# Performance work log

Hardware: AMD Instinct MI355X
Metric: run time of the kernel (lower is better)

## Reference

```python
import jax, jax.numpy as jnp
import numpy as np

M, K, N = 4096, 4096, 8192

def setup_inputs() -> dict:
    key = jax.random.key(0)
    k1, k2, k3 = jax.random.split(key, 3)
    a = jax.random.randint(k1, (M, K), -128, 128, dtype=jnp.int32).astype(jnp.int8)
    b = jax.random.randint(k2, (K, N), -128, 128, dtype=jnp.int32).astype(jnp.int8)
    scale = jax.random.uniform(k3, (N,), dtype=jnp.float32, minval=0.001, maxval=0.01)
    return {"a": a, "b": b, "scale": scale}

def reference(a, b, scale):
    acc = jax.lax.dot(a, b, preferred_element_type=jnp.int32)  # [M, N] int32
    return acc.astype(jnp.float32) * scale[None, :]  # [M, N] fp32
```

## Files before the change

kernel.cpp:

```cpp
#include <hip/hip_runtime.h>
#include <cstdint>
#include <cstddef>

#define M_DIM 4096
#define K_DIM 4096
#define N_DIM 8192

typedef int v4i __attribute__((ext_vector_type(4)));

__device__ __forceinline__ void load_lds16(const void* g, void* l) {
  __builtin_amdgcn_global_load_lds(
      (const __attribute__((address_space(1))) void*)g,
      (__attribute__((address_space(3))) void*)l,
      16, 0, 0);
}

__device__ __forceinline__ uint32_t pack4(int4 v) {
  return ((uint32_t)v.x & 0xFFu) | (((uint32_t)v.y & 0xFFu) << 8) |
         (((uint32_t)v.z & 0xFFu) << 16) | ((uint32_t)v.w << 24);
}

__global__ __launch_bounds__(256) void pack_a_kernel(const int* __restrict__ A32,
                                                     uint8_t* __restrict__ A8) {
  const int n16 = (M_DIM * K_DIM) / 16;
  const int stride = gridDim.x * 256;
  for (int i = blockIdx.x * 256 + threadIdx.x; i < n16; i += stride) {
    const int4* src = reinterpret_cast<const int4*>(A32) + (size_t)i * 4;
    int4 o;
    o.x = (int)pack4(src[0]);
    o.y = (int)pack4(src[1]);
    o.z = (int)pack4(src[2]);
    o.w = (int)pack4(src[3]);
    reinterpret_cast<int4*>(A8)[i] = o;
  }
}

#define TPITCH 132
__global__ __launch_bounds__(256) void pack_bt_kernel(const int* __restrict__ B32,
                                                      uint8_t* __restrict__ Bt) {
  __shared__ uint8_t tile[128 * TPITCH];
  const int t = threadIdx.x;
  const int n0 = blockIdx.x * 128;
  const int k0 = blockIdx.y * 128;

#pragma unroll
  for (int c = 0; c < 16; ++c) {
    const int chunk = c * 256 + t;
    const int row = chunk >> 5;
    const int nc4 = (chunk & 31);
    const int4 v = *reinterpret_cast<const int4*>(
        B32 + (size_t)(k0 + row) * N_DIM + n0 + nc4 * 4);
    *reinterpret_cast<uint32_t*>(&tile[row * TPITCH + nc4 * 4]) = pack4(v);
  }
  __syncthreads();

  const int nb = (t & 31) << 2;
  const int kc = (t >> 5) << 4;
  uint32_t dw[16];
#pragma unroll
  for (int j = 0; j < 16; ++j)
    dw[j] = *reinterpret_cast<const uint32_t*>(&tile[(kc + j) * TPITCH + nb]);

#pragma unroll
  for (int np = 0; np < 4; ++np) {
    const uint32_t sel = (uint32_t)np | (((uint32_t)np + 4u) << 8);
    uint32_t o[4];
#pragma unroll
    for (int d = 0; d < 4; ++d) {
      const uint32_t p01 = __builtin_amdgcn_perm(dw[4 * d + 1], dw[4 * d + 0], sel);
      const uint32_t p23 = __builtin_amdgcn_perm(dw[4 * d + 3], dw[4 * d + 2], sel);
      o[d] = __builtin_amdgcn_perm(p23, p01, 0x05040100u);
    }
    const int4 v = make_int4((int)o[0], (int)o[1], (int)o[2], (int)o[3]);
    *reinterpret_cast<int4*>(Bt + (size_t)(n0 + nb + np) * K_DIM + k0 + kc) = v;
  }
}

__global__ __launch_bounds__(256) void gemm_i8_kernel(const uint8_t* __restrict__ A,
                                                      const uint8_t* __restrict__ Bt,
                                                      const float* __restrict__ scale,
                                                      float* __restrict__ C) {
  __shared__ uint8_t sA[2][128 * 64];
  __shared__ uint8_t sB[2][128 * 64];

  const int t = threadIdx.x;
  const int lane = t & 63;
  const int wave = t >> 6;
  const int wr = wave >> 1;
  const int wc = wave & 1;
  const int lr = lane & 15;
  const int kh = lane >> 4;

  const int m0 = blockIdx.y * 128;
  const int n0 = blockIdx.x * 128;

  const int chunk0 = t;
  const int chunk1 = 256 + t;
  const int r0 = chunk0 >> 2, c0 = (chunk0 & 3) << 4;
  const int r1 = chunk1 >> 2, c1 = (chunk1 & 3) << 4;
  const uint8_t* a0 = A + (size_t)(m0 + r0) * K_DIM + c0;
  const uint8_t* a1 = A + (size_t)(m0 + r1) * K_DIM + c1;
  const uint8_t* b0 = Bt + (size_t)(n0 + r0) * K_DIM + c0;
  const uint8_t* b1 = Bt + (size_t)(n0 + r1) * K_DIM + c1;

  v4i acc[4][4];
#pragma unroll
  for (int i = 0; i < 4; ++i)
#pragma unroll
    for (int j = 0; j < 4; ++j)
      acc[i][j] = (v4i){0, 0, 0, 0};

  const int aoffBase = (wr * 64 + lr) * 64 + kh * 16;
  const int boffBase = (wc * 64 + lr) * 64 + kh * 16;

  load_lds16(a0, &sA[0][chunk0 * 16]);
  load_lds16(a1, &sA[0][chunk1 * 16]);
  load_lds16(b0, &sB[0][chunk0 * 16]);
  load_lds16(b1, &sB[0][chunk1 * 16]);
  __syncthreads();

  int cur = 0;
  const int NK = K_DIM / 64;
  for (int kt = 0; kt < NK; ++kt) {
    if (kt + 1 < NK) {
      const int ko = (kt + 1) * 64;
      load_lds16(a0 + ko, &sA[cur ^ 1][chunk0 * 16]);
      load_lds16(a1 + ko, &sA[cur ^ 1][chunk1 * 16]);
      load_lds16(b0 + ko, &sB[cur ^ 1][chunk0 * 16]);
      load_lds16(b1 + ko, &sB[cur ^ 1][chunk1 * 16]);
    }

    v4i af[4], bf[4];
#pragma unroll
    for (int mi = 0; mi < 4; ++mi)
      af[mi] = *reinterpret_cast<const v4i*>(&sA[cur][aoffBase + mi * 16 * 64]);
#pragma unroll
    for (int ni = 0; ni < 4; ++ni)
      bf[ni] = *reinterpret_cast<const v4i*>(&sB[cur][boffBase + ni * 16 * 64]);

#pragma unroll
    for (int mi = 0; mi < 4; ++mi)
#pragma unroll
      for (int ni = 0; ni < 4; ++ni)
        acc[mi][ni] = __builtin_amdgcn_mfma_i32_16x16x64_i8(af[mi], bf[ni], acc[mi][ni], 0, 0, 0);

    __syncthreads();
    cur ^= 1;
  }

  const int row0 = m0 + wr * 64 + kh * 4;
  const int col0 = n0 + wc * 64 + lr;
#pragma unroll
  for (int ni = 0; ni < 4; ++ni) {
    const int col = col0 + ni * 16;
    const float s = scale[col];
#pragma unroll
    for (int mi = 0; mi < 4; ++mi) {
#pragma unroll
      for (int r = 0; r < 4; ++r) {
        const int row = row0 + mi * 16 + r;
        C[(size_t)row * N_DIM + col] = (float)acc[mi][ni][r] * s;
      }
    }
  }
}

__global__ __launch_bounds__(256) void gemm_fallback(const int* __restrict__ A,
                                                     const int* __restrict__ B,
                                                     const float* __restrict__ scale,
                                                     float* __restrict__ C) {
  const int col = blockIdx.x * 16 + (threadIdx.x & 15);
  const int row = blockIdx.y * 16 + (threadIdx.x >> 4);
  int acc = 0;
  for (int k = 0; k < K_DIM; k += 4) {
    const int4 a = *reinterpret_cast<const int4*>(&A[(size_t)row * K_DIM + k]);
    acc += a.x * B[(size_t)(k + 0) * N_DIM + col];
    acc += a.y * B[(size_t)(k + 1) * N_DIM + col];
    acc += a.z * B[(size_t)(k + 2) * N_DIM + col];
    acc += a.w * B[(size_t)(k + 3) * N_DIM + col];
  }
  C[(size_t)row * N_DIM + col] = (float)acc * scale[col];
}

extern "C" void kernel_launch(void* const* d_in, const int* in_sizes, int n_in,
                              void* d_out, int out_size, void* d_ws, size_t ws_size,
                              hipStream_t stream) {
  const int* A32 = (const int*)d_in[0];
  const int* B32 = (const int*)d_in[1];
  const float* scale = (const float*)d_in[2];
  float* C = (float*)d_out;

  const size_t btBytes = (size_t)K_DIM * N_DIM;
  const size_t a8Bytes = (size_t)M_DIM * K_DIM;
  if (ws_size >= btBytes + a8Bytes) {
    uint8_t* Bt = (uint8_t*)d_ws;
    uint8_t* A8 = (uint8_t*)d_ws + btBytes;
    pack_a_kernel<<<2048, 256, 0, stream>>>(A32, A8);
    pack_bt_kernel<<<dim3(N_DIM / 128, K_DIM / 128), 256, 0, stream>>>(B32, Bt);
    gemm_i8_kernel<<<dim3(N_DIM / 128, M_DIM / 128), 256, 0, stream>>>(
        A8, Bt, scale, C);
  } else {
    gemm_fallback<<<dim3(N_DIM / 16, M_DIM / 16), 256, 0, stream>>>(
        A32, B32, scale, C);
  }
}
```

Measured before the change: 435.1 us.

## Rewrite int8 GEMM as 256x256 tiled, 8-wave, swizzled-LDS pipelined kernel

The int8 GEMM moves from 128x128 tiles with 4 waves and K-step 64 to 256x256 tiles with 8 waves and K-step 128. It adds an XOR-swizzled LDS layout against bank conflicts, a block-index remap for L2 locality, and a hand-scheduled pipeline that interleaves global-to-LDS staging with MFMA clusters using explicit vmcnt waits, barriers and setprio. The pack_bt kernel's thread-to-(k,n) mapping is also changed to improve write coalescing. The manual waitcnt and barrier schedule is fragile and uses a large LDS footprint (128 KB per block), so occupancy is limited.

```diff
diff --git a/kernel.cpp b/kernel.cpp
--- a/kernel.cpp
+++ b/kernel.cpp
@@ -5,6 +5,7 @@
 #define M_DIM 4096
 #define K_DIM 4096
 #define N_DIM 8192
+#define NKT (K_DIM / 128)
 
 typedef int v4i __attribute__((ext_vector_type(4)));
 
@@ -14,6 +15,15 @@
       (__attribute__((address_space(3))) void*)l,
       16, 0, 0);
 }
+
+#define FENCE() asm volatile("" ::: "memory")
+#define BARRIER()                      \
+  do {                                 \
+    FENCE();                           \
+    __builtin_amdgcn_s_barrier();      \
+    FENCE();                           \
+  } while (0)
+#define VMCNT(n) asm volatile("s_waitcnt vmcnt(" #n ")" ::: "memory")
 
 __device__ __forceinline__ uint32_t pack4(int4 v) {
   return ((uint32_t)v.x & 0xFFu) | (((uint32_t)v.y & 0xFFu) << 8) |
@@ -54,8 +64,8 @@
   }
   __syncthreads();
 
-  const int nb = (t & 31) << 2;
-  const int kc = (t >> 5) << 4;
+  const int kc = (t & 7) << 4;
+  const int nb = (t >> 3) << 2;
   uint32_t dw[16];
 #pragma unroll
   for (int j = 0; j < 16; ++j)
@@ -76,93 +86,144 @@
   }
 }
 
-__global__ __launch_bounds__(256) void gemm_i8_kernel(const uint8_t* __restrict__ A,
-                                                      const uint8_t* __restrict__ Bt,
-                                                      const float* __restrict__ scale,
-                                                      float* __restrict__ C) {
-  __shared__ uint8_t sA[2][128 * 64];
-  __shared__ uint8_t sB[2][128 * 64];
-
-  const int t = threadIdx.x;
-  const int lane = t & 63;
-  const int wave = t >> 6;
-  const int wr = wave >> 1;
-  const int wc = wave & 1;
-  const int lr = lane & 15;
-  const int kh = lane >> 4;
-
-  const int m0 = blockIdx.y * 128;
-  const int n0 = blockIdx.x * 128;
-
-  const int chunk0 = t;
-  const int chunk1 = 256 + t;
-  const int r0 = chunk0 >> 2, c0 = (chunk0 & 3) << 4;
-  const int r1 = chunk1 >> 2, c1 = (chunk1 & 3) << 4;
-  const uint8_t* a0 = A + (size_t)(m0 + r0) * K_DIM + c0;
-  const uint8_t* a1 = A + (size_t)(m0 + r1) * K_DIM + c1;
-  const uint8_t* b0 = Bt + (size_t)(n0 + r0) * K_DIM + c0;
-  const uint8_t* b1 = Bt + (size_t)(n0 + r1) * K_DIM + c1;
-
-  v4i acc[4][4];
-#pragma unroll
-  for (int i = 0; i < 4; ++i)
-#pragma unroll
-    for (int j = 0; j < 4; ++j)
-      acc[i][j] = (v4i){0, 0, 0, 0};
-
-  const int aoffBase = (wr * 64 + lr) * 64 + kh * 16;
-  const int boffBase = (wc * 64 + lr) * 64 + kh * 16;
-
-  load_lds16(a0, &sA[0][chunk0 * 16]);
-  load_lds16(a1, &sA[0][chunk1 * 16]);
-  load_lds16(b0, &sB[0][chunk0 * 16]);
-  load_lds16(b1, &sB[0][chunk1 * 16]);
-  __syncthreads();
-
-  int cur = 0;
-  const int NK = K_DIM / 64;
-  for (int kt = 0; kt < NK; ++kt) {
-    if (kt + 1 < NK) {
-      const int ko = (kt + 1) * 64;
-      load_lds16(a0 + ko, &sA[cur ^ 1][chunk0 * 16]);
-      load_lds16(a1 + ko, &sA[cur ^ 1][chunk1 * 16]);
-      load_lds16(b0 + ko, &sB[cur ^ 1][chunk0 * 16]);
-      load_lds16(b1 + ko, &sB[cur ^ 1][chunk1 * 16]);
-    }
-
-    v4i af[4], bf[4];
-#pragma unroll
-    for (int mi = 0; mi < 4; ++mi)
-      af[mi] = *reinterpret_cast<const v4i*>(&sA[cur][aoffBase + mi * 16 * 64]);
-#pragma unroll
-    for (int ni = 0; ni < 4; ++ni)
-      bf[ni] = *reinterpret_cast<const v4i*>(&sB[cur][boffBase + ni * 16 * 64]);
-
-#pragma unroll
-    for (int mi = 0; mi < 4; ++mi)
-#pragma unroll
-      for (int ni = 0; ni < 4; ++ni)
-        acc[mi][ni] = __builtin_amdgcn_mfma_i32_16x16x64_i8(af[mi], bf[ni], acc[mi][ni], 0, 0, 0);
-
-    __syncthreads();
-    cur ^= 1;
-  }
-
-  const int row0 = m0 + wr * 64 + kh * 4;
-  const int col0 = n0 + wc * 64 + lr;
+__global__ __launch_bounds__(512, 2) void gemm_i8_kernel(
+    const uint8_t* __restrict__ A, const uint8_t* __restrict__ Bt,
+    const float* __restrict__ scale, float* __restrict__ C) {
+  __shared__ uint8_t lds[2][2][2][128 * 128];
+
+  const int tid = threadIdx.x;
+  const int l = tid & 63;
+  const int wave = tid >> 6;
+  const int wr = wave >> 2;
+  const int wc = wave & 3;
+
+  int lin = blockIdx.y * (N_DIM / 256) + blockIdx.x;
+  lin = (lin & 7) * 64 + (lin >> 3);
+  const int bx = lin & 31;
+  const int by = lin >> 5;
+  const int m0 = by * 256;
+  const int n0 = bx * 256;
+
+  const int r0 = tid >> 3;
+  const int r1 = (512 + tid) >> 3;
+  const int s0 = tid & 7;
+  const int c0 = ((s0 ^ (r0 & 7)) << 4);
+  const int c1 = ((s0 ^ (r1 & 7)) << 4);
+  const uint8_t* Abase = A + (size_t)m0 * K_DIM;
+  const uint8_t* Bbase = Bt + (size_t)n0 * K_DIM;
+
+#define STAGE(OP, BASE, BUF, HALF, T)                                                \
+  do {                                                                               \
+    load_lds16((BASE) + (size_t)((HALF)*128 + r0) * K_DIM + (T)*128 + c0,            \
+               &lds[BUF][OP][HALF][tid * 16]);                                       \
+    load_lds16((BASE) + (size_t)((HALF)*128 + r1) * K_DIM + (T)*128 + c1,            \
+               &lds[BUF][OP][HALF][(512 + tid) * 16]);                               \
+  } while (0)
+
+  const int rb = (l & 15) * 128;
+  const int aswz0 = (((0 * 4 + (l >> 4)) ^ (l & 7)) << 4);
+  const int aswz1 = (((1 * 4 + (l >> 4)) ^ (l & 7)) << 4);
+  const int brb = ((wc & 1) * 64) * 128;
+
+  v4i acc[8][4];
+#pragma unroll
+  for (int i = 0; i < 8; ++i)
+#pragma unroll
+    for (int j = 0; j < 4; ++j) acc[i][j] = (v4i){0, 0, 0, 0};
+
+  STAGE(0, Abase, 0, 0, 0);
+  STAGE(0, Abase, 0, 1, 0);
+  STAGE(1, Bbase, 0, 0, 0);
+  STAGE(1, Bbase, 0, 1, 0);
+  STAGE(1, Bbase, 1, 0, 1);
+  STAGE(1, Bbase, 1, 1, 1);
+  VMCNT(4);
+  BARRIER();
+
+#define MFMA_CLUSTER(MB, NB)                                                        \
+  do {                                                                              \
+    __builtin_amdgcn_s_setprio(1);                                                  \
+    _Pragma("unroll") for (int mi = 0; mi < 4; ++mi)                                \
+        _Pragma("unroll") for (int ni = 0; ni < 2; ++ni) {                          \
+      acc[(MB)*4 + mi][(NB)*2 + ni] = __builtin_amdgcn_mfma_i32_16x16x64_i8(        \
+          aF[mi][0], bF[(NB)*2 + ni][0], acc[(MB)*4 + mi][(NB)*2 + ni], 0, 0, 0);   \
+      acc[(MB)*4 + mi][(NB)*2 + ni] = __builtin_amdgcn_mfma_i32_16x16x64_i8(        \
+          aF[mi][1], bF[(NB)*2 + ni][1], acc[(MB)*4 + mi][(NB)*2 + ni], 0, 0, 0);   \
+    }                                                                               \
+    __builtin_amdgcn_s_setprio(0);                                                  \
+    __builtin_amdgcn_sched_barrier(0);                                              \
+  } while (0)
+
+#define DO_TILE(T, BUF)                                                             \
+  do {                                                                              \
+    const int TA = ((T) + 1 < NKT) ? (T) + 1 : NKT - 1;     \
+    const int TB = ((T) + 2 < NKT) ? (T) + 2 : NKT - 1;      \
+    const uint8_t* _As = &lds[BUF][0][wr][0];                                       \
+    const uint8_t* _Bs = &lds[BUF][1][wc >> 1][0];                                  \
+    v4i aF[4][2];                                                                   \
+    v4i bF[4][2];                                                                   \
+                 \
+    _Pragma("unroll") for (int mi = 0; mi < 4; ++mi) {                              \
+      aF[mi][0] = *(const v4i*)&_As[mi * 2048 + rb + aswz0];                        \
+      aF[mi][1] = *(const v4i*)&_As[mi * 2048 + rb + aswz1];                        \
+    }                                                                               \
+    _Pragma("unroll") for (int ni = 0; ni < 2; ++ni) {                              \
+      bF[ni][0] = *(const v4i*)&_Bs[brb + ni * 2048 + rb + aswz0];                  \
+      bF[ni][1] = *(const v4i*)&_Bs[brb + ni * 2048 + rb + aswz1];                  \
+    }                                                                               \
+    STAGE(0, Abase, (BUF) ^ 1, 0, TA);                                              \
+    BARRIER();                                                                      \
+    MFMA_CLUSTER(0, 0);                                                             \
+    BARRIER();                                                                      \
+                           \
+    _Pragma("unroll") for (int ni = 2; ni < 4; ++ni) {                              \
+      bF[ni][0] = *(const v4i*)&_Bs[brb + ni * 2048 + rb + aswz0];                  \
+      bF[ni][1] = *(const v4i*)&_Bs[brb + ni * 2048 + rb + aswz1];                  \
+    }                                                                               \
+    STAGE(0, Abase, (BUF) ^ 1, 1, TA);                                              \
+    BARRIER();                                                                      \
+    MFMA_CLUSTER(0, 1);                                                             \
+    BARRIER();                                                                      \
+                           \
+    _Pragma("unroll") for (int mi = 0; mi < 4; ++mi) {                              \
+      aF[mi][0] = *(const v4i*)&_As[(4 + mi) * 2048 + rb + aswz0];                  \
+      aF[mi][1] = *(const v4i*)&_As[(4 + mi) * 2048 + rb + aswz1];                  \
+    }                                                                               \
+    STAGE(1, Bbase, BUF, 0, TB);                                                    \
+    BARRIER();                                                                      \
+    MFMA_CLUSTER(1, 0);                                                             \
+    BARRIER();                                                                      \
+         \
+    VMCNT(2);                                                                       \
+    STAGE(1, Bbase, BUF, 1, TB);                                                    \
+    BARRIER();                                                                      \
+    MFMA_CLUSTER(1, 1);                                                             \
+    BARRIER();                                                                      \
+  } while (0)
+
+  for (int t = 0; t < NKT; t += 2) {
+    DO_TILE(t, 0);
+    DO_TILE(t + 1, 1);
+  }
+
+  const int csub = (l >> 4) * 4;
+  const int colb = n0 + wc * 64 + (l & 15);
+  float* Cw = C + (size_t)(m0 + wr * 128) * N_DIM + colb;
 #pragma unroll
   for (int ni = 0; ni < 4; ++ni) {
-    const int col = col0 + ni * 16;
-    const float s = scale[col];
-#pragma unroll
-    for (int mi = 0; mi < 4; ++mi) {
+    const float s = scale[colb + ni * 16];
+#pragma unroll
+    for (int mi = 0; mi < 8; ++mi) {
 #pragma unroll
       for (int r = 0; r < 4; ++r) {
-        const int row = row0 + mi * 16 + r;
-        C[(size_t)row * N_DIM + col] = (float)acc[mi][ni][r] * s;
+        Cw[(size_t)(mi * 16 + csub + r) * N_DIM + ni * 16] =
+            (float)acc[mi][ni][r] * s;
       }
     }
   }
+#undef DO_TILE
+#undef MFMA_CLUSTER
+#undef STAGE
 }
 
 __global__ __launch_bounds__(256) void gemm_fallback(const int* __restrict__ A,
@@ -197,7 +258,7 @@
     uint8_t* A8 = (uint8_t*)d_ws + btBytes;
     pack_a_kernel<<<2048, 256, 0, stream>>>(A32, A8);
     pack_bt_kernel<<<dim3(N_DIM / 128, K_DIM / 128), 256, 0, stream>>>(B32, Bt);
-    gemm_i8_kernel<<<dim3(N_DIM / 128, M_DIM / 128), 256, 0, stream>>>(
+    gemm_i8_kernel<<<dim3(N_DIM / 256, M_DIM / 256), 512, 0, stream>>>(
         A8, Bt, scale, C);
   } else {
     gemm_fallback<<<dim3(N_DIM / 16, M_DIM / 16), 256, 0, stream>>>(
```

New measurement: 388.2 us. -10.8%, faster.
